# Optimization experiments

Hardware: AMD Instinct MI355X
Metric: run time of the kernel (lower is better)

Reference implementation:

```python
import jax, jax.numpy as jnp
import numpy as np

START_DISP = 0
DISP_NUM = 192
B, C, H, W = 2, 1, 384, 1248


def setup_inputs() -> dict:
    key = jax.random.key(0)
    k1, k2 = jax.random.split(key)
    left = jax.random.normal(k1, (B, C, H, W), dtype=jnp.float32)
    right = jax.random.normal(k2, (B, C, H, W), dtype=jnp.float32)
    return {"left_img": left, "right_img": right}


def _gen_cost(left, right):
    # left, right: [B,1,H,W] -> cost: [B,D,H,W]
    Wd = left.shape[-1]
    l = left[:, 0]   # [B,H,W]
    r = right[:, 0]  # [B,H,W]
    disp = jnp.arange(START_DISP, START_DISP + DISP_NUM)          # [D]
    idx = jnp.arange(Wd)[None, :] - disp[:, None]                 # [D,W] source col in right
    valid = (idx >= 0) & (idx < Wd)                               # region written by the torch loop
    r_shift = jnp.take(r, jnp.clip(idx, 0, Wd - 1), axis=-1)      # [B,H,D,W]
    r_shift = jnp.moveaxis(r_shift, 2, 1)                         # [B,D,H,W]
    cost = jnp.where(valid[None, :, None, :], l[:, None, :, :] * r_shift,
                     jnp.zeros((), dtype=l.dtype))
    return cost


def _regress(cost):
    disp_values = jnp.arange(START_DISP, START_DISP + DISP_NUM,
                             dtype=cost.dtype).reshape(1, -1, 1, 1)
    return jnp.sum(cost * disp_values, axis=1)  # [B,H,W]


def reference(left_img, right_img):
    cost = _gen_cost(left_img, right_img)
    return _regress(cost)
```

## Files before the change

kernel.cpp:

```cpp
#include <hip/hip_runtime.h>


#define WID 1248
#define DISP 192
#define KOUT 5
#define THREADS 256
#define NROWS 768

__global__ __launch_bounds__(THREADS) void stereo_row_kernel(
    const float* __restrict__ left,
    const float* __restrict__ right,
    float* __restrict__ out)
{
    __shared__ float r_pad[DISP + WID + 8];

    const int row = blockIdx.x;
    const long base = (long)row * WID;
    const int tid = threadIdx.x;

    for (int i = tid; i < DISP; i += THREADS) r_pad[i] = 0.0f;
    if (tid < 8) r_pad[DISP + WID + tid] = 0.0f;
    for (int i = tid; i < WID; i += THREADS) r_pad[DISP + i] = right[base + i];
    __syncthreads();

    const int w0 = tid * KOUT;
    if (w0 >= WID) return;

    float A = 0.0f, Bs = 0.0f;
    const int jstart = w0 - (DISP - 1);
    #pragma unroll 4
    for (int i = 0; i < DISP; ++i) {
        float rj = r_pad[DISP + jstart + i];
        float jf = (float)(jstart + i);
        A += rj;
        Bs = fmaf(jf, rj, Bs);
    }

    {
        float S = fmaf((float)w0, A, -Bs);
        out[base + w0] = left[base + w0] * S;
    }

    #pragma unroll
    for (int k = 1; k < KOUT; ++k) {
        const int w = w0 + k;
        float rn = r_pad[DISP + w];
        float ro = r_pad[w];
        A += rn - ro;
        Bs += (float)w * rn - (float)(w - DISP) * ro;
        if (w < WID) {
            float S = fmaf((float)w, A, -Bs);
            out[base + w] = left[base + w] * S;
        }
    }
}

extern "C" void kernel_launch(void* const* d_in, const int* in_sizes, int n_in,
                              void* d_out, int out_size, void* d_ws, size_t ws_size,
                              hipStream_t stream) {
    const float* left  = (const float*)d_in[0];
    const float* right = (const float*)d_in[1];
    float* out = (float*)d_out;
    stereo_row_kernel<<<dim3(NROWS), dim3(THREADS), 0, stream>>>(left, right, out);
}
```

Measured before the change: 63.35 us.

## Replace per-thread window sums with prefix-scan over row segments

Each row is now split into four segments handled by separate blocks. Within a block, shuffle-based and cross-wave prefix scans produce running sums of right[j] and a locally indexed weighted sum, and each output is computed from differences of two prefix entries. This replaces the per-thread 192-iteration windowed loop plus sliding updates, removing serial LDS reads and giving four times as many blocks. The cost is redundant loading of the overlapping 191-element halo for each segment. Float prefix differences may also round differently from the direct sums.

```diff
diff --git a/kernel.cpp b/kernel.cpp
--- a/kernel.cpp
+++ b/kernel.cpp
@@ -3,55 +3,74 @@
 
 #define WID 1248
 #define DISP 192
-#define KOUT 5
+#define SEG 312
 #define THREADS 256
 #define NROWS 768
 
-__global__ __launch_bounds__(THREADS) void stereo_row_kernel(
+__global__ __launch_bounds__(THREADS) void stereo_scan_kernel(
     const float* __restrict__ left,
     const float* __restrict__ right,
     float* __restrict__ out)
 {
-    __shared__ float r_pad[DISP + WID + 8];
+    __shared__ float Ps[520];
+    __shared__ float Qs[520];
+    __shared__ float wsS[4], wsQ[4];
 
-    const int row = blockIdx.x;
+    const int bid = blockIdx.x;
+    const int row = bid >> 2;
+    const int seg = bid & 3;
+    const int wstart = seg * SEG;
     const long base = (long)row * WID;
     const int tid = threadIdx.x;
+    const int lane = tid & 63;
+    const int wv = tid >> 6;
 
-    for (int i = tid; i < DISP; i += THREADS) r_pad[i] = 0.0f;
-    if (tid < 8) r_pad[DISP + WID + tid] = 0.0f;
-    for (int i = tid; i < WID; i += THREADS) r_pad[DISP + i] = right[base + i];
+    const int i0 = 2 * tid;
+    const int j0 = wstart - (DISP - 1) + i0;
+    float e0 = (j0     >= 0 && j0     < WID) ? right[base + j0]     : 0.0f;
+    float e1 = (j0 + 1 >= 0 && j0 + 1 < WID) ? right[base + j0 + 1] : 0.0f;
+
+    float s = e0 + e1;
+    float q = fmaf((float)i0, e0, (float)(i0 + 1) * e1);
+    const float ls = s, lq = q;
+
+    #pragma unroll
+    for (int d = 1; d < 64; d <<= 1) {
+        float ts = __shfl_up(s, (unsigned)d, 64);
+        float tq = __shfl_up(q, (unsigned)d, 64);
+        if (lane >= d) { s += ts; q += tq; }
+    }
+    if (lane == 63) { wsS[wv] = s; wsQ[wv] = q; }
     __syncthreads();
 
-    const int w0 = tid * KOUT;
-    if (w0 >= WID) return;
+    float offS = 0.0f, offQ = 0.0f;
+    if (wv > 0) { offS += wsS[0]; offQ += wsQ[0]; }
+    if (wv > 1) { offS += wsS[1]; offQ += wsQ[1]; }
+    if (wv > 2) { offS += wsS[2]; offQ += wsQ[2]; }
 
-    float A = 0.0f, Bs = 0.0f;
-    const int jstart = w0 - (DISP - 1);
-    #pragma unroll 4
-    for (int i = 0; i < DISP; ++i) {
-        float rj = r_pad[DISP + jstart + i];
-        float jf = (float)(jstart + i);
-        A += rj;
-        Bs = fmaf(jf, rj, Bs);
-    }
+    const float exS = offS + s - ls;
+    const float exQ = offQ + q - lq;
+    Ps[i0]     = exS;
+    Ps[i0 + 1] = exS + e0;
+    Qs[i0]     = exQ;
+    Qs[i0 + 1] = fmaf((float)i0, e0, exQ);
+    __syncthreads();
 
     {
-        float S = fmaf((float)w0, A, -Bs);
-        out[base + w0] = left[base + w0] * S;
+        const int t = tid;
+        const float A  = Ps[t + DISP] - Ps[t];
+        const float Qw = Qs[t + DISP] - Qs[t];
+        const float S  = fmaf((float)(t + DISP - 1), A, -Qw);
+        const int w = wstart + t;
+        out[base + w] = left[base + w] * S;
     }
-
-    #pragma unroll
-    for (int k = 1; k < KOUT; ++k) {
-        const int w = w0 + k;
-        float rn = r_pad[DISP + w];
-        float ro = r_pad[w];
-        A += rn - ro;
-        Bs += (float)w * rn - (float)(w - DISP) * ro;
-        if (w < WID) {
-            float S = fmaf((float)w, A, -Bs);
-            out[base + w] = left[base + w] * S;
-        }
+    if (tid < SEG - THREADS) {
+        const int t = THREADS + tid;
+        const float A  = Ps[t + DISP] - Ps[t];
+        const float Qw = Qs[t + DISP] - Qs[t];
+        const float S  = fmaf((float)(t + DISP - 1), A, -Qw);
+        const int w = wstart + t;
+        out[base + w] = left[base + w] * S;
     }
 }
 
@@ -61,5 +80,5 @@
     const float* left  = (const float*)d_in[0];
     const float* right = (const float*)d_in[1];
     float* out = (float*)d_out;
-    stereo_row_kernel<<<dim3(NROWS), dim3(THREADS), 0, stream>>>(left, right, out);
+    stereo_scan_kernel<<<dim3(NROWS * 4), dim3(THREADS), 0, stream>>>(left, right, out);
 }
```

Result: faster. 61.91 us (-2.3%).
